# Performance work log

Hardware: AMD Instinct MI355X
Metric: run time of the kernel (lower is better)

## Reference

```python
import jax, jax.numpy as jnp
import numpy as np

N_NODES = 100_000
N_EDGES = 1_600_000
IN_CH = 128
HIDDEN = 48
OUT_CH = 16
NEG_SLOPE = 0.2  # PyG GATConv default LeakyReLU slope


def setup_inputs() -> dict:
    key = jax.random.key(0)
    ks = jax.random.split(key, 8)
    x = jax.random.normal(ks[0], (N_NODES, IN_CH), dtype=jnp.float32)
    edge_index = jax.random.randint(ks[1], (2, N_EDGES), 0, N_NODES, dtype=jnp.int64)
    W = jax.random.normal(ks[2], (IN_CH, HIDDEN), dtype=jnp.float32) / np.sqrt(IN_CH)
    att_src = jax.random.normal(ks[3], (HIDDEN,), dtype=jnp.float32) / np.sqrt(HIDDEN)
    att_dst = jax.random.normal(ks[4], (HIDDEN,), dtype=jnp.float32) / np.sqrt(HIDDEN)
    gat_bias = jax.random.normal(ks[5], (HIDDEN,), dtype=jnp.float32) * 0.01
    lin_W = jax.random.normal(ks[6], (HIDDEN, OUT_CH), dtype=jnp.float32) / np.sqrt(HIDDEN)
    lin_b = jax.random.normal(ks[7], (OUT_CH,), dtype=jnp.float32) * 0.01
    return {"x": x, "edge_index": edge_index, "W": W, "att_src": att_src,
            "att_dst": att_dst, "gat_bias": gat_bias, "lin_W": lin_W, "lin_b": lin_b}


def reference(x, edge_index, W, att_src, att_dst, gat_bias, lin_W, lin_b):
    n = x.shape[0]
    # PyG GATConv adds self loops by default
    loops = jnp.arange(n, dtype=edge_index.dtype)
    src = jnp.concatenate([edge_index[0], loops])  # [E+N] message sources j
    dst = jnp.concatenate([edge_index[1], loops])  # [E+N] message targets i

    h = x @ W                      # [N, H] transformed node features
    a_src = h @ att_src            # [N] per-node source attention term
    a_dst = h @ att_dst            # [N] per-node destination attention term

    logits = jax.nn.leaky_relu(a_src[src] + a_dst[dst], NEG_SLOPE)  # [E+N]
    # segment softmax over incoming edges of each destination node
    m = jax.ops.segment_max(logits, dst, num_segments=n)            # [N]
    e = jnp.exp(logits - m[dst])
    denom = jax.ops.segment_sum(e, dst, num_segments=n)             # [N] (>0: self loop)
    alpha = e / denom[dst]                                          # [E+N]

    agg = jax.ops.segment_sum(h[src] * alpha[:, None], dst, num_segments=n)
    out = jax.nn.elu(agg + gat_bias)          # [N, H]
    # dropout is identity in eval mode
    z = out @ lin_W + lin_b                   # [N, OUT]
    return jax.nn.log_softmax(z, axis=-1)
```

## Files before the change

### kernel.cpp

```cpp
#include <hip/hip_runtime.h>
#include <hip/hip_fp16.h>

#define IN_CH 128
#define HID 48
#define OUT_CH 16
#define NEG_SLOPE 0.2f
#define SCAN_ELEMS 2048
#define ROWB 128

__device__ __forceinline__ float leaky(float x) { return x >= 0.f ? x : NEG_SLOPE * x; }
__device__ __forceinline__ float elu(float x) { return x > 0.f ? x : __expf(x) - 1.f; }

__device__ __forceinline__ void load_edge(const void* ei, int E, int is64, int e,
                                          int& s, int& d) {
    if (is64) {
        const long long* p = (const long long*)ei;
        s = (int)p[e];
        d = (int)p[(size_t)E + e];
    } else {
        const int* p = (const int*)ei;
        s = p[e];
        d = p[(size_t)E + e];
    }
}

__global__ void k_detect(const unsigned* __restrict__ ei, int* __restrict__ flag) {
    if (threadIdx.x == 0 && blockIdx.x == 0) {
        unsigned s = 0;
        for (int i = 1; i < 128; i += 2) s |= ei[i];
        *flag = (s == 0) ? 1 : 0;
    }
}

#define BLK_NODES 256
__global__ __launch_bounds__(256, 2) void k_xw(const float* __restrict__ x,
                                               const float* __restrict__ W,
                                               const float* __restrict__ att_src,
                                               const float* __restrict__ att_dst,
                                               __half* __restrict__ h2,
                                               float* __restrict__ a_src,
                                               float* __restrict__ a_dst,
                                               int* __restrict__ deg, int N) {
    __shared__ float Wl[IN_CH * HID];
    __shared__ float xl[BLK_NODES * 33];
    const int t = threadIdx.x;
    for (int i = t; i < IN_CH * HID / 4; i += 256)
        ((float4*)Wl)[i] = ((const float4*)W)[i];
    const int n0 = blockIdx.x * BLK_NODES;
    const int kq = t & 3;
    const int ng = t >> 2;
    const int k0 = kq * 12;

    float acc[4][12];
#pragma unroll
    for (int i = 0; i < 4; ++i)
#pragma unroll
        for (int j = 0; j < 12; ++j) acc[i][j] = 0.f;

    for (int c0 = 0; c0 < IN_CH; c0 += 32) {
        __syncthreads();
#pragma unroll
        for (int p = 0; p < 8; ++p) {
            int id = t + p * 256;
            int row = id >> 3;
            int seg = id & 7;
            int n = n0 + row;
            float4 v = make_float4(0.f, 0.f, 0.f, 0.f);
            if (n < N) v = ((const float4*)(x + (size_t)n * IN_CH + c0))[seg];
            float* dst = &xl[row * 33 + seg * 4];
            dst[0] = v.x; dst[1] = v.y; dst[2] = v.z; dst[3] = v.w;
        }
        __syncthreads();
#pragma unroll 8
        for (int cc = 0; cc < 32; ++cc) {
            int c = c0 + cc;
            float xv[4];
#pragma unroll
            for (int i = 0; i < 4; ++i) xv[i] = xl[(ng * 4 + i) * 33 + cc];
            const float* wr = &Wl[c * HID + k0];
#pragma unroll
            for (int j = 0; j < 12; ++j) {
                float wv = wr[j];
#pragma unroll
                for (int i = 0; i < 4; ++i) acc[i][j] += xv[i] * wv;
            }
        }
    }
#pragma unroll
    for (int i = 0; i < 4; ++i) {
        int n = n0 + ng * 4 + i;
        if (n < N) {
            uint* dst = (uint*)((char*)h2 + (size_t)n * ROWB) + k0 / 2;
#pragma unroll
            for (int j = 0; j < 6; ++j) {
                __half2 hv = __floats2half2_rn(acc[i][2 * j], acc[i][2 * j + 1]);
                dst[j] = *(const uint*)&hv;
            }
        }
    }
#pragma unroll
    for (int p = 0; p < 8; ++p) {
        int id = t + p * 256;
        int row = id >> 3;
        int seg = id & 7;
        int n = n0 + row;
        if (n < N) ((uint*)((char*)h2 + (size_t)n * ROWB))[24 + seg] = 0u;
    }
    float as_[4], ad_[4];
#pragma unroll
    for (int i = 0; i < 4; ++i) {
        float s1 = 0.f, s2 = 0.f;
#pragma unroll
        for (int j = 0; j < 12; ++j) {
            float a = acc[i][j];
            s1 += a * att_src[k0 + j];
            s2 += a * att_dst[k0 + j];
        }
        s1 += __shfl_xor(s1, 1); s1 += __shfl_xor(s1, 2);
        s2 += __shfl_xor(s2, 1); s2 += __shfl_xor(s2, 2);
        as_[i] = s1; ad_[i] = s2;
    }
    if (kq == 0) {
#pragma unroll
        for (int i = 0; i < 4; ++i) {
            int n = n0 + ng * 4 + i;
            if (n < N) { a_src[n] = as_[i]; a_dst[n] = ad_[i]; }
        }
    }
    {
        int n = n0 + t;
        if (n < N) deg[n] = 0;
    }
}

__global__ __launch_bounds__(256) void k_count(const void* __restrict__ ei,
                                               const int* __restrict__ flag,
                                               int* __restrict__ deg,
                                               unsigned short* __restrict__ rank, int E) {
    int e = blockIdx.x * blockDim.x + threadIdx.x;
    if (e >= E) return;
    int d = (*flag) ? (int)((const long long*)ei)[(size_t)E + e]
                    : ((const int*)ei)[(size_t)E + e];
    rank[e] = (unsigned short)atomicAdd(&deg[d], 1);
}

__global__ __launch_bounds__(256) void k_scan_block(const int* __restrict__ deg,
                                                    int* __restrict__ rowptr,
                                                    int* __restrict__ bsum, int N) {
    __shared__ int sm[256];
    const int t = threadIdx.x;
    const int base = blockIdx.x * SCAN_ELEMS + t * 8;
    int v[8];
    int s = 0;
#pragma unroll
    for (int i = 0; i < 8; ++i) {
        v[i] = (base + i < N) ? deg[base + i] : 0;
        s += v[i];
    }
    sm[t] = s;
    __syncthreads();
    for (int off = 1; off < 256; off <<= 1) {
        int y = (t >= off) ? sm[t - off] : 0;
        __syncthreads();
        sm[t] += y;
        __syncthreads();
    }
    int run = sm[t] - s;
#pragma unroll
    for (int i = 0; i < 8; ++i) {
        if (base + i < N) rowptr[base + i] = run;
        run += v[i];
    }
    if (t == 255) bsum[blockIdx.x] = sm[255];
}

__global__ __launch_bounds__(256) void k_scan_add(int* __restrict__ rowptr,
                                                  const int* __restrict__ bsum, int N, int E) {
    __shared__ int soff;
    const int chunk = (int)(((long long)blockIdx.x * 256) / SCAN_ELEMS);
    if (threadIdx.x == 0) {
        int run = 0;
        for (int b = 0; b < chunk; ++b) run += bsum[b];
        soff = run;
    }
    __syncthreads();
    int i = blockIdx.x * 256 + threadIdx.x;
    if (i == 0) rowptr[N] = E;
    if (i >= N) return;
    rowptr[i] += soff;
}

__global__ __launch_bounds__(256) void k_scatter(const void* __restrict__ ei,
                                                 const int* __restrict__ flag,
                                                 const int* __restrict__ rowptr,
                                                 const unsigned short* __restrict__ rank,
                                                 unsigned* __restrict__ srcs, int E) {
    int e = blockIdx.x * blockDim.x + threadIdx.x;
    if (e >= E) return;
    int is64 = *flag;
    int s, d;
    load_edge(ei, E, is64, e, s, d);
    int pos = rowptr[d] + (int)rank[e];
    __builtin_nontemporal_store((unsigned)s, srcs + pos);
}

__global__ __launch_bounds__(256) void k_gat_node(const int* __restrict__ rowptr,
                                                  const unsigned* __restrict__ srcs,
                                                  const float* __restrict__ a_src,
                                                  const float* __restrict__ a_dst,
                                                  const __half* __restrict__ h2,
                                                  const float* __restrict__ gat_bias,
                                                  const float* __restrict__ lin_W,
                                                  const float* __restrict__ lin_b,
                                                  float* __restrict__ out, int N) {
    __shared__ float Wl[HID * 17];
    __shared__ float lb[OUT_CH];
    __shared__ float gb[HID];
    __shared__ float o_sm[4][HID];
    const int t = threadIdx.x;
    for (int i = t; i < HID * OUT_CH; i += 256) Wl[(i >> 4) * 17 + (i & 15)] = lin_W[i];
    if (t < OUT_CH) lb[t] = lin_b[t];
    if (t >= 64 && t < 64 + HID) gb[t - 64] = gat_bias[t - 64];
    __syncthreads();

    const int wv = t >> 6;
    const int lane = t & 63;
    const int slot = lane >> 4;
    const int c = lane & 15;
    const int n = blockIdx.x * 4 + wv;
    const bool active = n < N;

    if (active) {
        const int base = rowptr[n];
        const int deg = rowptr[n + 1] - base;
        const float adn = a_dst[n];
        const float ev_self = __expf(fminf(leaky(a_src[n] + adn), 50.f));
        const char* hb = (const char*)h2;

        float a0 = 0.f, a1 = 0.f, a2 = 0.f, a3 = 0.f, evsum = 0.f;
        if (slot == 0) {
            evsum = ev_self;
            uint2 hv = *(const uint2*)(hb + (size_t)n * ROWB + 8 * c);
            float2 f0 = __half22float2(*(const __half2*)&hv.x);
            float2 f1 = __half22float2(*(const __half2*)&hv.y);
            a0 = ev_self * f0.x; a1 = ev_self * f0.y;
            a2 = ev_self * f1.x; a3 = ev_self * f1.y;
        }
        int j = slot;
#pragma unroll 2
        for (; j + 4 < deg; j += 8) {
            unsigned s0 = srcs[base + j];
            unsigned s1 = srcs[base + j + 4];
            float as0 = a_src[s0];
            float as1 = a_src[s1];
            uint2 hv0 = *(const uint2*)(hb + (size_t)s0 * ROWB + 8 * c);
            uint2 hv1 = *(const uint2*)(hb + (size_t)s1 * ROWB + 8 * c);
            float ev0 = __expf(fminf(leaky(as0 + adn), 50.f));
            float ev1 = __expf(fminf(leaky(as1 + adn), 50.f));
            float2 f00 = __half22float2(*(const __half2*)&hv0.x);
            float2 f01 = __half22float2(*(const __half2*)&hv0.y);
            float2 f10 = __half22float2(*(const __half2*)&hv1.x);
            float2 f11 = __half22float2(*(const __half2*)&hv1.y);
            evsum += ev0; evsum += ev1;
            a0 += ev0 * f00.x; a1 += ev0 * f00.y;
            a2 += ev0 * f01.x; a3 += ev0 * f01.y;
            a0 += ev1 * f10.x; a1 += ev1 * f10.y;
            a2 += ev1 * f11.x; a3 += ev1 * f11.y;
        }
        if (j < deg) {
            unsigned s0 = srcs[base + j];
            float as0 = a_src[s0];
            uint2 hv = *(const uint2*)(hb + (size_t)s0 * ROWB + 8 * c);
            float ev = __expf(fminf(leaky(as0 + adn), 50.f));
            float2 f0 = __half22float2(*(const __half2*)&hv.x);
            float2 f1 = __half22float2(*(const __half2*)&hv.y);
            evsum += ev;
            a0 += ev * f0.x; a1 += ev * f0.y;
            a2 += ev * f1.x; a3 += ev * f1.y;
        }
        evsum += __shfl_xor(evsum, 16); evsum += __shfl_xor(evsum, 32);
        a0 += __shfl_xor(a0, 16); a0 += __shfl_xor(a0, 32);
        a1 += __shfl_xor(a1, 16); a1 += __shfl_xor(a1, 32);
        a2 += __shfl_xor(a2, 16); a2 += __shfl_xor(a2, 32);
        a3 += __shfl_xor(a3, 16); a3 += __shfl_xor(a3, 32);
        const float inv = 1.f / evsum;
        if (slot == 0 && c < 12) {
            float4 v = make_float4(elu(a0 * inv + gb[4 * c + 0]),
                                   elu(a1 * inv + gb[4 * c + 1]),
                                   elu(a2 * inv + gb[4 * c + 2]),
                                   elu(a3 * inv + gb[4 * c + 3]));
            *(float4*)&o_sm[wv][4 * c] = v;
        }
    }
    __syncthreads();

    if (active) {
        const float* o = o_sm[wv];
        float z = 0.f;
#pragma unroll
        for (int i = 0; i < 12; ++i) {
            int k = 12 * slot + i;
            z += o[k] * Wl[k * 17 + c];
        }
        z += __shfl_xor(z, 16); z += __shfl_xor(z, 32);
        z += lb[c];
        float mx = z;
#pragma unroll
        for (int off = 8; off; off >>= 1) mx = fmaxf(mx, __shfl_xor(mx, off, 16));
        float ev = __expf(z - mx);
#pragma unroll
        for (int off = 8; off; off >>= 1) ev += __shfl_xor(ev, off, 16);
        float lse = mx + __logf(ev);
        if (slot == 0) out[(size_t)n * OUT_CH + c] = z - lse;
    }
}

extern "C" void kernel_launch(void* const* d_in, const int* in_sizes, int n_in,
                              void* d_out, int out_size, void* d_ws, size_t ws_size,
                              hipStream_t stream) {
    const float* x = (const float*)d_in[0];
    const void* edge_index = d_in[1];
    const float* W = (const float*)d_in[2];
    const float* att_src = (const float*)d_in[3];
    const float* att_dst = (const float*)d_in[4];
    const float* gat_bias = (const float*)d_in[5];
    const float* lin_W = (const float*)d_in[6];
    const float* lin_b = (const float*)d_in[7];
    float* out = (float*)d_out;

    const int N = in_sizes[0] / IN_CH;
    const int E = in_sizes[1] / 2;

    __half* h2 = (__half*)d_ws;
    float* a_src = (float*)((char*)d_ws + (size_t)N * ROWB);
    float* a_dst = a_src + N;
    int* rowptr = (int*)(a_dst + N);
    int* degbuf = rowptr + N + 1;
    int* bsum = degbuf + N;
    int* flag = bsum + 64;
    unsigned short* rank = (unsigned short*)(flag + 1);
    unsigned* srcs =
        (unsigned*)(((uintptr_t)(rank + E) + 3) & ~(uintptr_t)3);

    const int nodeBlocks = (N + 255) / 256;
    const int edgeBlocks = (E + 255) / 256;
    const int scanBlocks = (N + SCAN_ELEMS - 1) / SCAN_ELEMS;

    k_detect<<<1, 64, 0, stream>>>((const unsigned*)edge_index, flag);
    k_xw<<<(N + BLK_NODES - 1) / BLK_NODES, 256, 0, stream>>>(x, W, att_src, att_dst,
                                                              h2, a_src, a_dst, degbuf, N);
    k_count<<<edgeBlocks, 256, 0, stream>>>(edge_index, flag, degbuf, rank, E);
    k_scan_block<<<scanBlocks, 256, 0, stream>>>(degbuf, rowptr, bsum, N);
    k_scan_add<<<nodeBlocks, 256, 0, stream>>>(rowptr, bsum, N, E);
    k_scatter<<<edgeBlocks, 256, 0, stream>>>(edge_index, flag, rowptr, rank, srcs, E);
    k_gat_node<<<(N + 3) / 4, 256, 0, stream>>>(rowptr, srcs, a_src, a_dst,
                                                h2, gat_bias, lin_W, lin_b, out, N);
}
```

Before: 236.2 us.

## Compute edge weights once per wave lane and fold detect kernel into k_xw

The per-node gather loop now has all 64 lanes of a wave load source indices and compute attention exponentials together, one edge per lane. Each lane packs its (weight, src) pair into shared memory, and the 4 slots of 16 lanes then gather fp16 feature rows from that buffer. Before, each of the 16 channel lanes in a slot recomputed the same exp and a_src load, so this cuts redundant index loads, a_src gathers and exp calls. The separate single-thread edge-type detect kernel is merged into k_xw to save a launch. The change adds LDS traffic and a full-wave shuffle reduction, and relies on wave-synchronous LDS use with no explicit barrier.

```diff
diff --git a/kernel.cpp b/kernel.cpp
--- a/kernel.cpp
+++ b/kernel.cpp
@@ -24,26 +24,25 @@
     }
 }
 
-__global__ void k_detect(const unsigned* __restrict__ ei, int* __restrict__ flag) {
-    if (threadIdx.x == 0 && blockIdx.x == 0) {
-        unsigned s = 0;
-        for (int i = 1; i < 128; i += 2) s |= ei[i];
-        *flag = (s == 0) ? 1 : 0;
-    }
-}
-
 #define BLK_NODES 256
 __global__ __launch_bounds__(256, 2) void k_xw(const float* __restrict__ x,
                                                const float* __restrict__ W,
                                                const float* __restrict__ att_src,
                                                const float* __restrict__ att_dst,
+                                               const unsigned* __restrict__ ei,
                                                __half* __restrict__ h2,
                                                float* __restrict__ a_src,
                                                float* __restrict__ a_dst,
-                                               int* __restrict__ deg, int N) {
+                                               int* __restrict__ deg,
+                                               int* __restrict__ flag, int N) {
     __shared__ float Wl[IN_CH * HID];
     __shared__ float xl[BLK_NODES * 33];
     const int t = threadIdx.x;
+    if (blockIdx.x == 0 && t == 0) {
+        unsigned sdet = 0;
+        for (int i = 1; i < 128; i += 2) sdet |= ei[i];
+        *flag = (sdet == 0) ? 1 : 0;
+    }
     for (int i = t; i < IN_CH * HID / 4; i += 256)
         ((float4*)Wl)[i] = ((const float4*)W)[i];
     const int n0 = blockIdx.x * BLK_NODES;
@@ -217,6 +216,7 @@
     __shared__ float lb[OUT_CH];
     __shared__ float gb[HID];
     __shared__ float o_sm[4][HID];
+    __shared__ unsigned long long evb[4][64];
     const int t = threadIdx.x;
     for (int i = t; i < HID * OUT_CH; i += 256) Wl[(i >> 4) * 17 + (i & 15)] = lin_W[i];
     if (t < OUT_CH) lb[t] = lin_b[t];
@@ -237,48 +237,44 @@
         const float ev_self = __expf(fminf(leaky(a_src[n] + adn), 50.f));
         const char* hb = (const char*)h2;
 
-        float a0 = 0.f, a1 = 0.f, a2 = 0.f, a3 = 0.f, evsum = 0.f;
+        float a0 = 0.f, a1 = 0.f, a2 = 0.f, a3 = 0.f;
+        float evsum = (lane == 0) ? ev_self : 0.f;
         if (slot == 0) {
-            evsum = ev_self;
             uint2 hv = *(const uint2*)(hb + (size_t)n * ROWB + 8 * c);
-            float2 f0 = __half22float2(*(const __half2*)&hv.x);
-            float2 f1 = __half22float2(*(const __half2*)&hv.y);
-            a0 = ev_self * f0.x; a1 = ev_self * f0.y;
-            a2 = ev_self * f1.x; a3 = ev_self * f1.y;
-        }
-        int j = slot;
-#pragma unroll 2
-        for (; j + 4 < deg; j += 8) {
-            unsigned s0 = srcs[base + j];
-            unsigned s1 = srcs[base + j + 4];
-            float as0 = a_src[s0];
-            float as1 = a_src[s1];
-            uint2 hv0 = *(const uint2*)(hb + (size_t)s0 * ROWB + 8 * c);
-            uint2 hv1 = *(const uint2*)(hb + (size_t)s1 * ROWB + 8 * c);
-            float ev0 = __expf(fminf(leaky(as0 + adn), 50.f));
-            float ev1 = __expf(fminf(leaky(as1 + adn), 50.f));
-            float2 f00 = __half22float2(*(const __half2*)&hv0.x);
-            float2 f01 = __half22float2(*(const __half2*)&hv0.y);
-            float2 f10 = __half22float2(*(const __half2*)&hv1.x);
-            float2 f11 = __half22float2(*(const __half2*)&hv1.y);
-            evsum += ev0; evsum += ev1;
-            a0 += ev0 * f00.x; a1 += ev0 * f00.y;
-            a2 += ev0 * f01.x; a3 += ev0 * f01.y;
-            a0 += ev1 * f10.x; a1 += ev1 * f10.y;
-            a2 += ev1 * f11.x; a3 += ev1 * f11.y;
-        }
-        if (j < deg) {
-            unsigned s0 = srcs[base + j];
-            float as0 = a_src[s0];
-            uint2 hv = *(const uint2*)(hb + (size_t)s0 * ROWB + 8 * c);
-            float ev = __expf(fminf(leaky(as0 + adn), 50.f));
-            float2 f0 = __half22float2(*(const __half2*)&hv.x);
-            float2 f1 = __half22float2(*(const __half2*)&hv.y);
+            __half2 h01 = *(const __half2*)&hv.x;
+            __half2 h23 = *(const __half2*)&hv.y;
+            a0 = ev_self * __low2float(h01);
+            a1 = ev_self * __high2float(h01);
+            a2 = ev_self * __low2float(h23);
+            a3 = ev_self * __high2float(h23);
+        }
+        for (int c0 = 0; c0 < deg; c0 += 64) {
+            int j = c0 + lane;
+            unsigned s = 0;
+            float ev = 0.f;
+            if (j < deg) {
+                s = srcs[base + j];
+                ev = __expf(fminf(leaky(a_src[s] + adn), 50.f));
+            }
             evsum += ev;
-            a0 += ev * f0.x; a1 += ev * f0.y;
-            a2 += ev * f1.x; a3 += ev * f1.y;
-        }
-        evsum += __shfl_xor(evsum, 16); evsum += __shfl_xor(evsum, 32);
+            evb[wv][lane] = ((unsigned long long)__float_as_uint(ev) << 32) | s;
+            const int cnt = (deg - c0 < 64) ? (deg - c0) : 64;
+#pragma unroll 4
+            for (int jj = slot; jj < cnt; jj += 4) {
+                unsigned long long pr = evb[wv][jj];
+                unsigned sj = (unsigned)pr;
+                float evj = __uint_as_float((unsigned)(pr >> 32));
+                uint2 hv = *(const uint2*)(hb + (size_t)sj * ROWB + 8 * c);
+                __half2 h01 = *(const __half2*)&hv.x;
+                __half2 h23 = *(const __half2*)&hv.y;
+                a0 += evj * __low2float(h01);
+                a1 += evj * __high2float(h01);
+                a2 += evj * __low2float(h23);
+                a3 += evj * __high2float(h23);
+            }
+        }
+#pragma unroll
+        for (int off = 1; off < 64; off <<= 1) evsum += __shfl_xor(evsum, off);
         a0 += __shfl_xor(a0, 16); a0 += __shfl_xor(a0, 32);
         a1 += __shfl_xor(a1, 16); a1 += __shfl_xor(a1, 32);
         a2 += __shfl_xor(a2, 16); a2 += __shfl_xor(a2, 32);
@@ -346,9 +342,9 @@
     const int edgeBlocks = (E + 255) / 256;
     const int scanBlocks = (N + SCAN_ELEMS - 1) / SCAN_ELEMS;
 
-    k_detect<<<1, 64, 0, stream>>>((const unsigned*)edge_index, flag);
-    k_xw<<<(N + BLK_NODES - 1) / BLK_NODES, 256, 0, stream>>>(x, W, att_src, att_dst,
-                                                              h2, a_src, a_dst, degbuf, N);
+    k_xw<<<(N + BLK_NODES - 1) / BLK_NODES, 256, 0, stream>>>(
+        x, W, att_src, att_dst, (const unsigned*)edge_index,
+        h2, a_src, a_dst, degbuf, flag, N);
     k_count<<<edgeBlocks, 256, 0, stream>>>(edge_index, flag, degbuf, rank, E);
     k_scan_block<<<scanBlocks, 256, 0, stream>>>(degbuf, rowptr, bsum, N);
     k_scan_add<<<nodeBlocks, 256, 0, stream>>>(rowptr, bsum, N, E);
```

Result: no change. 233.6 us (-1.1%).
